# Kernel tuning notes

Hardware: AMD Instinct MI355X
Metric: run time of the kernel (lower is better)

The kernel has to match this reference:

```python
import jax, jax.numpy as jnp
import numpy as np

EPS = 1e-8
HALF_BIN = 0.1 / 2.0  # discretization_param / 2


def setup_inputs() -> dict:
    key = jax.random.key(0)
    k1, k2, k3, k4, k5, k6 = jax.random.split(key, 6)
    B, K = 4194304, 3
    predicted_purchase_prob = jax.random.uniform(k1, (B,), jnp.float32, 0.01, 0.99)
    mu = jax.random.normal(k2, (K, B), jnp.float32) * 5.0 + 10.0
    sigma = jax.random.uniform(k3, (K, B), jnp.float32, 0.1, 2.0)
    weight = jax.random.uniform(k4, (K, B), jnp.float32, 0.0, 1.0)
    paid = jax.random.uniform(k5, (B,)) > 0.5
    vals = jax.random.uniform(k6, (B,), jnp.float32, 0.1, 50.0)
    true_values = jnp.where(paid, vals, 0.0)
    return {
        "predicted_purchase_prob": predicted_purchase_prob,
        "mu": mu,
        "sigma": sigma,
        "weight": weight,
        "true_values": true_values,
    }


def reference(predicted_purchase_prob, mu, sigma, weight, true_values):
    p = predicted_purchase_prob  # [B]
    targets = (true_values > 0).astype(p.dtype)  # [B]
    # BCE with torch-style log clamping at -100
    log_p = jnp.clip(jnp.log(p + 0.0), -100.0)
    log_1mp = jnp.clip(jnp.log(1.0 - p), -100.0)
    purchase_loss = -jnp.mean(targets * log_p + (1.0 - targets) * log_1mp)

    # Mixture-of-logistics discretized likelihood, vectorized over [K, B]
    inv_s = 1.0 / (sigma + EPS)  # [K, B]
    tv = true_values[None, :]  # [1, B]
    cdf_upper = jax.nn.sigmoid((tv + HALF_BIN - mu) * inv_s)
    cdf_lower = jax.nn.sigmoid((tv - HALF_BIN - mu) * inv_s)
    prob_density = jnp.maximum(cdf_upper - cdf_lower, EPS)  # clamp(min=1e-8)
    likelihood = jnp.sum(weight * prob_density, axis=0)  # [B]
    log_likelihood = jnp.log(likelihood + EPS)  # [B]

    paid_mask = true_values > 0
    n_paid = jnp.sum(paid_mask.astype(p.dtype))
    ll_sum = jnp.sum(jnp.where(paid_mask, log_likelihood, 0.0))
    ltv_loss = -jnp.where(n_paid > 0, ll_sum / jnp.maximum(n_paid, 1.0), 0.0)

    return purchase_loss + ltv_loss
```

## Files before the change

kernel.cpp:

```cpp
#include <hip/hip_runtime.h>
#include <math.h>

#define EPS 1e-8f
#define HALF_BIN 0.05f

__device__ __forceinline__ float sigmoid_diff(float xu, float xl) {
    float eu = __expf(fminf(-xu, 87.0f));
    float el = __expf(fminf(-xl, 87.0f));
    float num = el - eu;
    float den = (1.0f + eu) * (1.0f + el);
    return __fdividef(num, den);
}

template <int K>
__device__ __forceinline__ void process_group_buf(
    const float4 (&buf)[3 * K + 2],
    float& bce, float& ll, float& npaid)
{
    float pv[4] = {buf[0].x, buf[0].y, buf[0].z, buf[0].w};
    float t [4] = {buf[1].x, buf[1].y, buf[1].z, buf[1].w};
    float lik[4] = {0.0f, 0.0f, 0.0f, 0.0f};

    #pragma unroll
    for (int k = 0; k < K; ++k) {
        const float4 mf = buf[2 + 3 * k];
        const float4 sf = buf[3 + 3 * k];
        const float4 wf = buf[4 + 3 * k];
        float m[4] = {mf.x, mf.y, mf.z, mf.w};
        float s[4] = {sf.x, sf.y, sf.z, sf.w};
        float w[4] = {wf.x, wf.y, wf.z, wf.w};
        #pragma unroll
        for (int j = 0; j < 4; ++j) {
            float inv_s = __fdividef(1.0f, s[j] + EPS);
            float xu = (t[j] + HALF_BIN - m[j]) * inv_s;
            float xl = (t[j] - HALF_BIN - m[j]) * inv_s;
            float pd = fmaxf(sigmoid_diff(xu, xl), EPS);
            lik[j] = fmaf(w[j], pd, lik[j]);
        }
    }

    #pragma unroll
    for (int j = 0; j < 4; ++j) {
        bool paid = t[j] > 0.0f;
        float val = paid ? pv[j] : (1.0f - pv[j]);
        bce -= fmaxf(__logf(val), -100.0f);
        float lg = __logf(lik[j] + EPS);
        ll    += paid ? lg : 0.0f;
        npaid += paid ? 1.0f : 0.0f;
    }
}

template <int K>
__device__ __forceinline__ void process_elem(
    float pv, float t, const float* mu, const float* sigma, const float* weight,
    size_t i, size_t B, float& bce, float& ll, float& npaid)
{
    float lik = 0.0f;
    #pragma unroll
    for (int k = 0; k < K; ++k) {
        size_t off = (size_t)k * B + i;
        float inv_s = __fdividef(1.0f, sigma[off] + EPS);
        float xu = (t + HALF_BIN - mu[off]) * inv_s;
        float xl = (t - HALF_BIN - mu[off]) * inv_s;
        float pd = fmaxf(sigmoid_diff(xu, xl), EPS);
        lik = fmaf(weight[off], pd, lik);
    }
    bool paid = t > 0.0f;
    float val = paid ? pv : (1.0f - pv);
    bce -= fmaxf(__logf(val), -100.0f);
    float lg = __logf(lik + EPS);
    ll    += paid ? lg : 0.0f;
    npaid += paid ? 1.0f : 0.0f;
}

template <int K>
__global__ __launch_bounds__(256, 4) void zimol_main(
    const float* __restrict__ p,
    const float* __restrict__ mu,
    const float* __restrict__ sigma,
    const float* __restrict__ weight,
    const float* __restrict__ tv,
    float* __restrict__ part_bce,
    float* __restrict__ part_ll,
    float* __restrict__ part_n,
    int B)
{
    const int tid    = blockIdx.x * blockDim.x + threadIdx.x;
    const int stride = gridDim.x * blockDim.x;

    float bce = 0.0f, ll = 0.0f, npaid = 0.0f;

    if ((B & 3) == 0) {
        const int B4 = B >> 2;
        const float4* __restrict__ p4  = (const float4*)p;
        const float4* __restrict__ tv4 = (const float4*)tv;
        const float4* __restrict__ mu4 = (const float4*)mu;
        const float4* __restrict__ sg4 = (const float4*)sigma;
        const float4* __restrict__ wt4 = (const float4*)weight;

        constexpr int NB = 3 * K + 2;
        int i = tid;
        for (; i + stride < B4; i += 2 * stride) {
            float4 buf[2][NB];
            #pragma unroll
            for (int u = 0; u < 2; ++u) {
                const int idx = i + u * stride;
                buf[u][0] = p4[idx];
                buf[u][1] = tv4[idx];
                #pragma unroll
                for (int k = 0; k < K; ++k) {
                    const size_t off = (size_t)k * (size_t)B4;
                    buf[u][2 + 3 * k] = mu4[off + idx];
                    buf[u][3 + 3 * k] = sg4[off + idx];
                    buf[u][4 + 3 * k] = wt4[off + idx];
                }
            }
            process_group_buf<K>(buf[0], bce, ll, npaid);
            process_group_buf<K>(buf[1], bce, ll, npaid);
        }
        for (; i < B4; i += stride) {
            float4 buf[NB];
            buf[0] = p4[i];
            buf[1] = tv4[i];
            #pragma unroll
            for (int k = 0; k < K; ++k) {
                const size_t off = (size_t)k * (size_t)B4;
                buf[2 + 3 * k] = mu4[off + i];
                buf[3 + 3 * k] = sg4[off + i];
                buf[4 + 3 * k] = wt4[off + i];
            }
            process_group_buf<K>(buf, bce, ll, npaid);
        }
    } else {
        for (int i = tid; i < B; i += stride) {
            process_elem<K>(p[i], tv[i], mu, sigma, weight,
                            (size_t)i, (size_t)B, bce, ll, npaid);
        }
    }

    #pragma unroll
    for (int off = 32; off > 0; off >>= 1) {
        bce   += __shfl_down(bce,   off, 64);
        ll    += __shfl_down(ll,    off, 64);
        npaid += __shfl_down(npaid, off, 64);
    }

    __shared__ float sdata[3][4];
    const int wave = threadIdx.x >> 6;
    const int lane = threadIdx.x & 63;
    if (lane == 0) {
        sdata[0][wave] = bce;
        sdata[1][wave] = ll;
        sdata[2][wave] = npaid;
    }
    __syncthreads();
    if (threadIdx.x == 0) {
        float b = 0.0f, l = 0.0f, n = 0.0f;
        #pragma unroll
        for (int w = 0; w < 4; ++w) {
            b += sdata[0][w];
            l += sdata[1][w];
            n += sdata[2][w];
        }
        part_bce[blockIdx.x] = b;
        part_ll [blockIdx.x] = l;
        part_n  [blockIdx.x] = n;
    }
}

__global__ __launch_bounds__(256) void zimol_reduce(
    const float* __restrict__ part_bce,
    const float* __restrict__ part_ll,
    const float* __restrict__ part_n,
    float* __restrict__ out, int nblocks, int B)
{
    double b = 0.0, l = 0.0, n = 0.0;
    for (int i = threadIdx.x; i < nblocks; i += 256) {
        b += (double)part_bce[i];
        l += (double)part_ll[i];
        n += (double)part_n[i];
    }
    #pragma unroll
    for (int off = 32; off > 0; off >>= 1) {
        b += __shfl_down(b, off, 64);
        l += __shfl_down(l, off, 64);
        n += __shfl_down(n, off, 64);
    }
    __shared__ double sdata[3][4];
    const int wave = threadIdx.x >> 6;
    const int lane = threadIdx.x & 63;
    if (lane == 0) {
        sdata[0][wave] = b;
        sdata[1][wave] = l;
        sdata[2][wave] = n;
    }
    __syncthreads();
    if (threadIdx.x == 0) {
        double tb = 0.0, tl = 0.0, tn = 0.0;
        #pragma unroll
        for (int w = 0; w < 4; ++w) {
            tb += sdata[0][w];
            tl += sdata[1][w];
            tn += sdata[2][w];
        }
        double purchase = tb / (double)B;
        double ltv = (tn > 0.0) ? -(tl / fmax(tn, 1.0)) : 0.0;
        out[0] = (float)(purchase + ltv);
    }
}

extern "C" void kernel_launch(void* const* d_in, const int* in_sizes, int n_in,
                              void* d_out, int out_size, void* d_ws, size_t ws_size,
                              hipStream_t stream) {
    const float* p      = (const float*)d_in[0];
    const float* mu     = (const float*)d_in[1];
    const float* sigma  = (const float*)d_in[2];
    const float* weight = (const float*)d_in[3];
    const float* tv     = (const float*)d_in[4];
    float* out = (float*)d_out;

    const int B = in_sizes[0];
    const int K = in_sizes[1] / B;

    const int threads = 256;
    int work = ((B + 3) >> 2);
    int blocks = (work + threads - 1) / threads;
    if (blocks > 2048) blocks = 2048;
    if (blocks < 1) blocks = 1;

    float* part_bce = (float*)d_ws;
    float* part_ll  = part_bce + blocks;
    float* part_n   = part_ll  + blocks;

    if (K == 3) {
        zimol_main<3><<<blocks, threads, 0, stream>>>(p, mu, sigma, weight, tv,
                                                      part_bce, part_ll, part_n, B);
    } else if (K == 1) {
        zimol_main<1><<<blocks, threads, 0, stream>>>(p, mu, sigma, weight, tv,
                                                      part_bce, part_ll, part_n, B);
    } else if (K == 2) {
        zimol_main<2><<<blocks, threads, 0, stream>>>(p, mu, sigma, weight, tv,
                                                      part_bce, part_ll, part_n, B);
    } else {
        zimol_main<4><<<blocks, threads, 0, stream>>>(p, mu, sigma, weight, tv,
                                                      part_bce, part_ll, part_n, B);
    }

    zimol_reduce<<<1, threads, 0, stream>>>(part_bce, part_ll, part_n, out, blocks, B);
}
```

Baseline: 196.8 us.

## Stage input tiles into LDS with async global_load_lds double buffering

Replaces the direct float4 register loads with async global-to-LDS copies (global_load_lds, 16 bytes per lane) into a double-buffered 512-element tile per stream, so the next tile is fetched while the current one is computed. Each block now handles a contiguous range of tiles instead of a grid-stride loop, and the grid shrinks to at most 768 blocks. LDS use per block grows to about 45 KB, and the launch-bounds occupancy hint is dropped. A __syncthreads per tile and LDS reads are added, and occupancy may fall. There is no wait on the async copies other than the barrier, which relies on the compiler inserting vmcnt waits.

```diff
diff --git a/kernel.cpp b/kernel.cpp
--- a/kernel.cpp
+++ b/kernel.cpp
@@ -3,6 +3,7 @@
 
 #define EPS 1e-8f
 #define HALF_BIN 0.05f
+#define TILE 512
 
 __device__ __forceinline__ float sigmoid_diff(float xu, float xl) {
     float eu = __expf(fminf(-xu, 87.0f));
@@ -12,42 +13,23 @@
     return __fdividef(num, den);
 }
 
-template <int K>
-__device__ __forceinline__ void process_group_buf(
-    const float4 (&buf)[3 * K + 2],
+__device__ __forceinline__ void gload_lds16(const float* gsrc, float* ldst) {
+    __builtin_amdgcn_global_load_lds(
+        (const __attribute__((address_space(1))) void*)gsrc,
+        (__attribute__((address_space(3))) void*)ldst,
+        16 , 0 , 0 );
+}
+
+__device__ __forceinline__ void elem_math(
+    float pvj, float tj, float lik,
     float& bce, float& ll, float& npaid)
 {
-    float pv[4] = {buf[0].x, buf[0].y, buf[0].z, buf[0].w};
-    float t [4] = {buf[1].x, buf[1].y, buf[1].z, buf[1].w};
-    float lik[4] = {0.0f, 0.0f, 0.0f, 0.0f};
-
-    #pragma unroll
-    for (int k = 0; k < K; ++k) {
-        const float4 mf = buf[2 + 3 * k];
-        const float4 sf = buf[3 + 3 * k];
-        const float4 wf = buf[4 + 3 * k];
-        float m[4] = {mf.x, mf.y, mf.z, mf.w};
-        float s[4] = {sf.x, sf.y, sf.z, sf.w};
-        float w[4] = {wf.x, wf.y, wf.z, wf.w};
-        #pragma unroll
-        for (int j = 0; j < 4; ++j) {
-            float inv_s = __fdividef(1.0f, s[j] + EPS);
-            float xu = (t[j] + HALF_BIN - m[j]) * inv_s;
-            float xl = (t[j] - HALF_BIN - m[j]) * inv_s;
-            float pd = fmaxf(sigmoid_diff(xu, xl), EPS);
-            lik[j] = fmaf(w[j], pd, lik[j]);
-        }
-    }
-
-    #pragma unroll
-    for (int j = 0; j < 4; ++j) {
-        bool paid = t[j] > 0.0f;
-        float val = paid ? pv[j] : (1.0f - pv[j]);
-        bce -= fmaxf(__logf(val), -100.0f);
-        float lg = __logf(lik[j] + EPS);
-        ll    += paid ? lg : 0.0f;
-        npaid += paid ? 1.0f : 0.0f;
-    }
+    bool paid = tj > 0.0f;
+    float val = paid ? pvj : (1.0f - pvj);
+    bce -= fmaxf(__logf(val), -100.0f);
+    float lg = __logf(lik + EPS);
+    ll    += paid ? lg : 0.0f;
+    npaid += paid ? 1.0f : 0.0f;
 }
 
 template <int K>
@@ -65,16 +47,11 @@
         float pd = fmaxf(sigmoid_diff(xu, xl), EPS);
         lik = fmaf(weight[off], pd, lik);
     }
-    bool paid = t > 0.0f;
-    float val = paid ? pv : (1.0f - pv);
-    bce -= fmaxf(__logf(val), -100.0f);
-    float lg = __logf(lik + EPS);
-    ll    += paid ? lg : 0.0f;
-    npaid += paid ? 1.0f : 0.0f;
+    elem_math(pv, t, lik, bce, ll, npaid);
 }
 
 template <int K>
-__global__ __launch_bounds__(256, 4) void zimol_main(
+__global__ __launch_bounds__(256) void zimol_main(
     const float* __restrict__ p,
     const float* __restrict__ mu,
     const float* __restrict__ sigma,
@@ -85,54 +62,82 @@
     float* __restrict__ part_n,
     int B)
 {
-    const int tid    = blockIdx.x * blockDim.x + threadIdx.x;
-    const int stride = gridDim.x * blockDim.x;
+    constexpr int NS = 3 * K + 2;
+    __shared__ __align__(16) float lds[2][NS][TILE];
+    __shared__ float sdata[3][4];
+
+    const int lane = threadIdx.x & 63;
+    const int wave = threadIdx.x >> 6;
+
+    const float* bases[NS];
+    bases[0] = p;
+    bases[1] = tv;
+    #pragma unroll
+    for (int k = 0; k < K; ++k) {
+        bases[2 + 3 * k] = mu     + (size_t)k * (size_t)B;
+        bases[3 + 3 * k] = sigma  + (size_t)k * (size_t)B;
+        bases[4 + 3 * k] = weight + (size_t)k * (size_t)B;
+    }
 
     float bce = 0.0f, ll = 0.0f, npaid = 0.0f;
 
-    if ((B & 3) == 0) {
-        const int B4 = B >> 2;
-        const float4* __restrict__ p4  = (const float4*)p;
-        const float4* __restrict__ tv4 = (const float4*)tv;
-        const float4* __restrict__ mu4 = (const float4*)mu;
-        const float4* __restrict__ sg4 = (const float4*)sigma;
-        const float4* __restrict__ wt4 = (const float4*)weight;
-
-        constexpr int NB = 3 * K + 2;
-        int i = tid;
-        for (; i + stride < B4; i += 2 * stride) {
-            float4 buf[2][NB];
+    const int ntiles = B / TILE;
+    const int tpb = (ntiles + gridDim.x - 1) / gridDim.x;
+    const int t0 = blockIdx.x * tpb;
+    const int t1 = (t0 + tpb < ntiles) ? (t0 + tpb) : ntiles;
+
+    auto stage = [&](int buf, int t) {
+        const int e0 = t * TILE;
+        #pragma unroll
+        for (int u = 0; u < 2 * NS; ++u) {
+            if ((u & 3) == wave) {
+                const int s = u >> 1;
+                const int h = u & 1;
+                gload_lds16(bases[s] + e0 + h * 256 + lane * 4,
+                            &lds[buf][s][h * 256]);
+            }
+        }
+    };
+
+    if (t0 < t1) {
+        stage(0, t0);
+        int cur = 0;
+        for (int t = t0; t < t1; ++t) {
+            __syncthreads();
+            if (t + 1 < t1) stage(cur ^ 1, t + 1);
+
+            const int e = threadIdx.x * 2;
+            const float2 pv = *(const float2*)&lds[cur][0][e];
+            const float2 tvv = *(const float2*)&lds[cur][1][e];
+            float lik0 = 0.0f, lik1 = 0.0f;
             #pragma unroll
-            for (int u = 0; u < 2; ++u) {
-                const int idx = i + u * stride;
-                buf[u][0] = p4[idx];
-                buf[u][1] = tv4[idx];
-                #pragma unroll
-                for (int k = 0; k < K; ++k) {
-                    const size_t off = (size_t)k * (size_t)B4;
-                    buf[u][2 + 3 * k] = mu4[off + idx];
-                    buf[u][3 + 3 * k] = sg4[off + idx];
-                    buf[u][4 + 3 * k] = wt4[off + idx];
+            for (int k = 0; k < K; ++k) {
+                const float2 m = *(const float2*)&lds[cur][2 + 3 * k][e];
+                const float2 s = *(const float2*)&lds[cur][3 + 3 * k][e];
+                const float2 w = *(const float2*)&lds[cur][4 + 3 * k][e];
+                {
+                    float inv_s = __fdividef(1.0f, s.x + EPS);
+                    float xu = (tvv.x + HALF_BIN - m.x) * inv_s;
+                    float xl = (tvv.x - HALF_BIN - m.x) * inv_s;
+                    lik0 = fmaf(w.x, fmaxf(sigmoid_diff(xu, xl), EPS), lik0);
+                }
+                {
+                    float inv_s = __fdividef(1.0f, s.y + EPS);
+                    float xu = (tvv.y + HALF_BIN - m.y) * inv_s;
+                    float xl = (tvv.y - HALF_BIN - m.y) * inv_s;
+                    lik1 = fmaf(w.y, fmaxf(sigmoid_diff(xu, xl), EPS), lik1);
                 }
             }
-            process_group_buf<K>(buf[0], bce, ll, npaid);
-            process_group_buf<K>(buf[1], bce, ll, npaid);
-        }
-        for (; i < B4; i += stride) {
-            float4 buf[NB];
-            buf[0] = p4[i];
-            buf[1] = tv4[i];
-            #pragma unroll
-            for (int k = 0; k < K; ++k) {
-                const size_t off = (size_t)k * (size_t)B4;
-                buf[2 + 3 * k] = mu4[off + i];
-                buf[3 + 3 * k] = sg4[off + i];
-                buf[4 + 3 * k] = wt4[off + i];
-            }
-            process_group_buf<K>(buf, bce, ll, npaid);
-        }
-    } else {
-        for (int i = tid; i < B; i += stride) {
+            elem_math(pv.x, tvv.x, lik0, bce, ll, npaid);
+            elem_math(pv.y, tvv.y, lik1, bce, ll, npaid);
+            cur ^= 1;
+        }
+    }
+
+    {
+        const int base = ntiles * TILE;
+        for (int i = base + blockIdx.x * blockDim.x + threadIdx.x; i < B;
+             i += gridDim.x * blockDim.x) {
             process_elem<K>(p[i], tv[i], mu, sigma, weight,
                             (size_t)i, (size_t)B, bce, ll, npaid);
         }
@@ -145,9 +150,6 @@
         npaid += __shfl_down(npaid, off, 64);
     }
 
-    __shared__ float sdata[3][4];
-    const int wave = threadIdx.x >> 6;
-    const int lane = threadIdx.x & 63;
     if (lane == 0) {
         sdata[0][wave] = bce;
         sdata[1][wave] = ll;
@@ -223,9 +225,14 @@
     const int K = in_sizes[1] / B;
 
     const int threads = 256;
-    int work = ((B + 3) >> 2);
-    int blocks = (work + threads - 1) / threads;
-    if (blocks > 2048) blocks = 2048;
+    int ntiles = B / TILE;
+    int blocks;
+    if (ntiles > 0) {
+        blocks = (ntiles < 768) ? ntiles : 768;
+    } else {
+        blocks = (B + threads - 1) / threads;
+        if (blocks > 768) blocks = 768;
+    }
     if (blocks < 1) blocks = 1;
 
     float* part_bce = (float*)d_ws;
```

Result: no change. 198.0 us (+0.6%).
